# Optimization experiments

Hardware: AMD Instinct MI355X
Metric: run time of the kernel (lower is better)

The kernel has to match this reference:

```python
import jax, jax.numpy as jnp
from jax import lax
import numpy as np

K_LIST = [2, 4, 8]

def setup_inputs() -> dict:
    key = jax.random.key(0)
    k1, k2 = jax.random.split(key)
    B_, C, H, Wd = 8, 256, 128, 128
    x = jax.random.normal(k1, (B_, C, H, Wd), dtype=jnp.float32)
    # conv weights init ~ N(0, 1e-6) per the module's 'zero' init, bias zero
    W = jax.random.normal(k2, (len(K_LIST), 1, C, 3, 3), dtype=jnp.float32) * 1e-6
    Bb = jnp.zeros((len(K_LIST), 1), dtype=jnp.float32)
    return {"x": x, "W": W, "B": Bb}


def _band_grid(h, w):
    # signed max of (fftfreq_h, rfftfreq_w) coords, matching torch code
    fh = jnp.fft.fftfreq(h).astype(jnp.float32)          # [h]
    fw = jnp.fft.rfftfreq(w).astype(jnp.float32)         # [w//2+1]
    return jnp.maximum(fh[:, None], fw[None, :])         # [h, w//2+1]


def reference(x, W, B):
    b, c, h, w = x.shape
    x_dtype = x.dtype
    x32 = x.astype(jnp.float32)
    x_fft = jnp.fft.rfft2(x32, norm='ortho')             # [b,c,h,w//2+1] complex
    grid = _band_grid(h, w)
    pre_x = x32
    out = jnp.zeros_like(x32)
    for idx, freq in enumerate(K_LIST):
        mask = (grid < 0.5 / freq).astype(jnp.float32)   # [h, w//2+1]
        low = jnp.fft.irfft2(x_fft * mask, s=(h, w), norm='ortho')
        high = pre_x - low
        pre_x = low
        # Conv2d(in=256, out=1, k=3, pad=1) on att_feat=x
        fwgt = lax.conv_general_dilated(
            x32, W[idx], window_strides=(1, 1), padding='SAME',
            dimension_numbers=('NCHW', 'OIHW', 'NCHW'))
        fwgt = fwgt + B[idx][None, :, None, None]        # [b,1,h,w]
        gate = jax.nn.sigmoid(fwgt) * 2.0
        out = out + gate * high                          # broadcast over channels
    out = out + pre_x                                    # residual low-frequency part
    return out.astype(x_dtype)
```

## Files before the change

kernel.cpp:

```cpp
#include <hip/hip_runtime.h>


#define NPIX 16384
#define NCHN 256

typedef __attribute__((ext_vector_type(8))) short bf16x8;
typedef __attribute__((ext_vector_type(4))) float f32x4;

__device__ __align__(16) short g_f[64][128];
__device__ __align__(16) short g_h[192][256];
__device__ __align__(16) short g_e[3][256][192];
__device__ __align__(16) short g_p[3][128][64];

static __device__ __forceinline__ short f2bf(float f) {
  unsigned u = __float_as_uint(f);
  unsigned r = (u + 0x7fffu + ((u >> 16) & 1u)) >> 16;
  return (short)r;
}
static __device__ __forceinline__ float bf2f(short s) {
  return __uint_as_float(((unsigned)(unsigned short)s) << 16);
}
static __device__ __forceinline__ f32x4 mfma16(bf16x8 a, bf16x8 b, f32x4 c) {
  return __builtin_amdgcn_mfma_f32_16x16x32_bf16(a, b, c, 0, 0, 0);
}

static __device__ void const_fill(int idx) {
  const float C = 6.2831853071795864769f / 128.f;
  if (idx < 8192) {
    int n = idx >> 7, q = idx & 127;
    int j = n & 31;
    float ang = C * (float)((j * q) & 127);
    float v = (n < 32) ? cosf(ang) : -sinf(ang);
    reinterpret_cast<short*>(g_f)[idx] = f2bf(v);
  } else if (idx < 57344) {
    int e = idx - 8192;
    int d = e >> 8, kk = e & 255;
    int r = (d < 96) ? d : d - 96;
    int ifr = (r < 32) ? r : r + 32;
    float ang = C * (float)((ifr * (kk & 127)) & 127);
    float cv = cosf(ang) * (1.f / 128.f), sv = sinf(ang) * (1.f / 128.f);
    float v = (d < 96) ? ((kk < 128) ? cv : sv) : ((kk < 128) ? -sv : cv);
    reinterpret_cast<short*>(g_h)[e] = f2bf(v);
  } else if (idx < 204800) {
    int e = idx - 57344;
    int k = e / 49152; int e2 = e % 49152;
    int mm = e2 / 192, kk = e2 % 192;
    int nk = 32 >> k;
    int r = (kk < 96) ? kk : kk - 96;
    bool allow = (r < nk) || (r >= 32);
    int ifr = (r < 32) ? r : r + 32;
    float ang = C * (float)((ifr * (mm & 127)) & 127);
    float cv = cosf(ang), sv = sinf(ang);
    float v = (mm < 128) ? ((kk < 96) ? cv : -sv) : ((kk < 96) ? sv : cv);
    reinterpret_cast<short*>(g_e)[e] = f2bf(allow ? v : 0.f);
  } else if (idx < 229376) {
    int e = idx - 204800;
    int k = e / 8192; int e2 = e % 8192;
    int n = e2 >> 6, jj = e2 & 63;
    int nk = 32 >> k;
    int j = jj & 31;
    bool valid = (j < nk) && (jj < 32 || j > 0);
    float wj = (j == 0) ? (1.f / 128.f) : (2.f / 128.f);
    float ang = C * (float)((j * n) & 127);
    float v = (jj < 32) ? (wj * cosf(ang)) : (-wj * sinf(ang));
    reinterpret_cast<short*>(g_p)[e] = f2bf(valid ? v : 0.f);
  }
}

__global__ __launch_bounds__(256) void gates_partial_kernel(
    const float* __restrict__ x, const float* __restrict__ Wg,
    float* __restrict__ partial, int nsplit) {
  int bid = blockIdx.x;
  int ngates = 512 * nsplit;
  if (bid >= ngates) {
    const_fill((bid - ngates) * 256 + threadIdx.x);
    return;
  }
  int b = bid & 7;
  int tile = (bid >> 3) & 63;
  int cs = bid >> 9;
  int chans = NCHN / nsplit;
  int m = ((tile >> 3) << 4) + (threadIdx.x >> 4);
  int n = ((tile & 7) << 4) + (threadIdx.x & 15);
  float a0 = 0.f, a1 = 0.f, a2 = 0.f;
  const float* xb = x + (size_t)b * NCHN * NPIX;
  for (int c = cs * chans; c < cs * chans + chans; ++c) {
    const float* xc = xb + (size_t)c * NPIX;
    const float* wc = Wg + c * 9;
    #pragma unroll
    for (int dh = -1; dh <= 1; ++dh) {
      int gm = m + dh;
      bool vm = (unsigned)gm < 128u;
      #pragma unroll
      for (int dw = -1; dw <= 1; ++dw) {
        int gn = n + dw;
        float xv = (vm && (unsigned)gn < 128u) ? xc[gm * 128 + gn] : 0.f;
        int tap = (dh + 1) * 3 + (dw + 1);
        a0 = fmaf(xv, wc[tap], a0);
        a1 = fmaf(xv, wc[2304 + tap], a1);
        a2 = fmaf(xv, wc[4608 + tap], a2);
      }
    }
  }
  int pix = m * 128 + n;
  float* pp = partial + (size_t)(cs * 8 + b) * 3 * NPIX;
  pp[pix]            = a0;
  pp[NPIX + pix]     = a1;
  pp[2 * NPIX + pix] = a2;
}

__global__ __launch_bounds__(256) void gates_combine_kernel(
    const float* __restrict__ partial, const float* __restrict__ Bg,
    short* __restrict__ dcoef, int nsplit) {
  int bid = blockIdx.x;
  int b = bid & 7;
  int px = (bid >> 3) * 256 + threadIdx.x;
  float a0 = Bg[0], a1 = Bg[1], a2 = Bg[2];
  for (int cs = 0; cs < nsplit; ++cs) {
    const float* pp = partial + (size_t)(cs * 8 + b) * 3 * NPIX;
    a0 += pp[px];
    a1 += pp[NPIX + px];
    a2 += pp[2 * NPIX + px];
  }
  float g1 = 2.f / (1.f + expf(-a0));
  float g2 = 2.f / (1.f + expf(-a1));
  float g3 = 2.f / (1.f + expf(-a2));
  int pix = b * NPIX + px;
  dcoef[pix]          = f2bf(g1 - 1.f);
  dcoef[131072 + pix] = f2bf(g2 - g1);
  dcoef[262144 + pix] = f2bf(g3 - g2);
  dcoef[393216 + pix] = f2bf(1.f - g3);
}

__global__ __launch_bounds__(256) void gates_kernel(
    const float* __restrict__ x, const float* __restrict__ Wg,
    const float* __restrict__ Bg, short* __restrict__ dcoef) {
  int blk = blockIdx.x;
  if (blk >= 512) {
    const_fill((blk - 512) * 256 + threadIdx.x);
    return;
  }
  int b = blk >> 6;
  int tile = blk & 63;
  int m = ((tile >> 3) << 4) + (threadIdx.x >> 4);
  int n = ((tile & 7) << 4) + (threadIdx.x & 15);
  float a0 = 0.f, a1 = 0.f, a2 = 0.f;
  const float* xb = x + (size_t)b * NCHN * NPIX;
  for (int c = 0; c < NCHN; ++c) {
    const float* xc = xb + (size_t)c * NPIX;
    const float* wc = Wg + c * 9;
    #pragma unroll
    for (int dh = -1; dh <= 1; ++dh) {
      int gm = m + dh;
      bool vm = (unsigned)gm < 128u;
      #pragma unroll
      for (int dw = -1; dw <= 1; ++dw) {
        int gn = n + dw;
        float xv = (vm && (unsigned)gn < 128u) ? xc[gm * 128 + gn] : 0.f;
        int tap = (dh + 1) * 3 + (dw + 1);
        a0 = fmaf(xv, wc[tap], a0);
        a1 = fmaf(xv, wc[2304 + tap], a1);
        a2 = fmaf(xv, wc[4608 + tap], a2);
      }
    }
  }
  a0 += Bg[0]; a1 += Bg[1]; a2 += Bg[2];
  float g1 = 2.f / (1.f + expf(-a0));
  float g2 = 2.f / (1.f + expf(-a1));
  float g3 = 2.f / (1.f + expf(-a2));
  int pix = b * NPIX + m * 128 + n;
  dcoef[pix]          = f2bf(g1 - 1.f);
  dcoef[131072 + pix] = f2bf(g2 - g1);
  dcoef[262144 + pix] = f2bf(g3 - g2);
  dcoef[393216 + pix] = f2bf(1.f - g3);
}

__global__ __launch_bounds__(512, 2) void fbm_kernel(
    const float* __restrict__ x, const short* __restrict__ dcoef,
    float* __restrict__ out) {
  __shared__ __align__(16) short Xs[16384];
  __shared__ __align__(16) short WVs[8192];
  __shared__ __align__(16) short Ds2[6144];
  char* XsB = reinterpret_cast<char*>(Xs);
  char* PlaneB = XsB;
  char* WsB = reinterpret_cast<char*>(WVs);
  char* DsB = reinterpret_cast<char*>(Ds2);

  int t = threadIdx.x;
  int bid = blockIdx.x;
  int b = bid >> 5;
  int cg = bid & 31;
  size_t img0 = ((size_t)b << 8) + ((size_t)cg << 3);
  int lane = t & 63, w = t >> 6;
  int l15 = lane & 15, l4 = lane >> 4;
  const f32x4 zero = {0.f, 0.f, 0.f, 0.f};

  const short4* d0p = reinterpret_cast<const short4*>(dcoef + ((size_t)b << 14));

  for (int c = 0; c < 8; ++c) {
    f32x4 oaccC[8];
    {
      const f32x4* xv4 = reinterpret_cast<const f32x4*>(x + (img0 + c) * NPIX);
      #pragma unroll
      for (int i = 0; i < 8; ++i) {
        int f = t + i * 512;
        f32x4 xv = __builtin_nontemporal_load(&xv4[f]);
        short4 dv = d0p[f];
        f32x4 dvf = {bf2f(dv.x), bf2f(dv.y), bf2f(dv.z), bf2f(dv.w)};
        oaccC[i] = xv + dvf * xv;
        int row = f >> 5;
        int byte = row * 256 + (((f & 31) * 8) ^ ((row & 7) << 4));
        short4 s;
        s.x = f2bf(xv[0]); s.y = f2bf(xv[1]); s.z = f2bf(xv[2]); s.w = f2bf(xv[3]);
        *reinterpret_cast<short4*>(XsB + byte) = s;
      }
    }
    __syncthreads();

    {
      int Ntile = w & 3, Mq = w >> 2;
      int n = Ntile * 16 + l15;
      f32x4 acc[4] = {zero, zero, zero, zero};
      #pragma unroll
      for (int ks = 0; ks < 4; ++ks) {
        int koff = ks * 32 + l4 * 8;
        bf16x8 bf = *reinterpret_cast<const bf16x8*>(&g_f[n][koff]);
        #pragma unroll
        for (int mt = 0; mt < 4; ++mt) {
          int p = (Mq * 4 + mt) * 16 + l15;
          bf16x8 a = *reinterpret_cast<const bf16x8*>(
              XsB + p * 256 + ((koff * 2) ^ ((p & 7) << 4)));
          acc[mt] = mfma16(a, bf, acc[mt]);
        }
      }
      #pragma unroll
      for (int mt = 0; mt < 4; ++mt) {
        int p0 = (Mq * 4 + mt) * 16 + l4 * 4;
        short4 s;
        s.x = f2bf(acc[mt][0]); s.y = f2bf(acc[mt][1]);
        s.z = f2bf(acc[mt][2]); s.w = f2bf(acc[mt][3]);
        *reinterpret_cast<short4*>(WsB + n * 256 + ((p0 * 2) ^ ((n & 7) << 4))) = s;
      }
    }
    __syncthreads();

    {
      int Ntile = w & 1, Mt3 = w >> 1;
      int n = Ntile * 16 + l15;
      f32x4 acc[3] = {zero, zero, zero};
      #pragma unroll
      for (int ks = 0; ks < 8; ++ks) {
        int koff = ks * 32 + l4 * 8;
        int wrow = n + ((ks >= 4) ? 32 : 0);
        bf16x8 bb = *reinterpret_cast<const bf16x8*>(
            WsB + wrow * 256 + (((koff & 127) * 2) ^ ((wrow & 7) << 4)));
        #pragma unroll
        for (int mt = 0; mt < 3; ++mt) {
          int d = (Mt3 * 3 + mt) * 16 + l15;
          bf16x8 aa = *reinterpret_cast<const bf16x8*>(&g_h[d][koff]);
          acc[mt] = mfma16(aa, bb, acc[mt]);
        }
      }
      #pragma unroll
      for (int mt = 0; mt < 3; ++mt) {
        int d0 = (Mt3 * 3 + mt) * 16 + l4 * 4;
        short4 s;
        s.x = f2bf(acc[mt][0]); s.y = f2bf(acc[mt][1]);
        s.z = f2bf(acc[mt][2]); s.w = f2bf(acc[mt][3]);
        *reinterpret_cast<short4*>(DsB + n * 384 + ((d0 * 2) ^ ((n & 7) << 4))) = s;
      }
    }
    __syncthreads();

    int Mg3 = w >> 2, Ng3 = w & 3;
    for (int k = 0; k < 3; ++k) {
      {
        f32x4 acc[2][2] = {{zero, zero}, {zero, zero}};
        #pragma unroll
        for (int ks = 0; ks < 6; ++ks) {
          int koff = ks * 32 + l4 * 8;
          bf16x8 b0 = *reinterpret_cast<const bf16x8*>(
              DsB + l15 * 384 + ((koff * 2) ^ ((l15 & 7) << 4)));
          int j1 = 16 + l15;
          bf16x8 b1 = *reinterpret_cast<const bf16x8*>(
              DsB + j1 * 384 + ((koff * 2) ^ ((j1 & 7) << 4)));
          #pragma unroll
          for (int mi = 0; mi < 2; ++mi) {
            int mstk = (2 * w + mi) * 16 + l15;
            bf16x8 aa = *reinterpret_cast<const bf16x8*>(&g_e[k][mstk][koff]);
            acc[mi][0] = mfma16(aa, b0, acc[mi][0]);
            acc[mi][1] = mfma16(aa, b1, acc[mi][1]);
          }
        }
        #pragma unroll
        for (int mi = 0; mi < 2; ++mi) {
          #pragma unroll
          for (int ni = 0; ni < 2; ++ni) {
            int j = ni * 16 + l15;
            #pragma unroll
            for (int r = 0; r < 4; ++r) {
              int mstk = (2 * w + mi) * 16 + l4 * 4 + r;
              int m = mstk & 127;
              int jst = ((mstk >> 7) << 5) + j;
              *reinterpret_cast<short*>(WsB + m * 128 + ((jst * 2) ^ ((m & 7) << 4))) =
                  f2bf(acc[mi][ni][r]);
            }
          }
        }
      }
      __syncthreads();
      {
        f32x4 acc[4][2] = {{zero, zero}, {zero, zero}, {zero, zero}, {zero, zero}};
        #pragma unroll
        for (int ks = 0; ks < 2; ++ks) {
          int koff = ks * 32 + l4 * 8;
          bf16x8 bfr[2];
          #pragma unroll
          for (int nt = 0; nt < 2; ++nt) {
            int nout = (Ng3 * 2 + nt) * 16 + l15;
            bfr[nt] = *reinterpret_cast<const bf16x8*>(&g_p[k][nout][koff]);
          }
          #pragma unroll
          for (int mt = 0; mt < 4; ++mt) {
            int m = (Mg3 * 4 + mt) * 16 + l15;
            bf16x8 aa = *reinterpret_cast<const bf16x8*>(
                WsB + m * 128 + ((koff * 2) ^ ((m & 7) << 4)));
            acc[mt][0] = mfma16(aa, bfr[0], acc[mt][0]);
            acc[mt][1] = mfma16(aa, bfr[1], acc[mt][1]);
          }
        }
        #pragma unroll
        for (int mt = 0; mt < 4; ++mt) {
          #pragma unroll
          for (int nt = 0; nt < 2; ++nt) {
            int col = (Ng3 * 2 + nt) * 16 + l15;
            #pragma unroll
            for (int r = 0; r < 4; ++r) {
              int row = (Mg3 * 4 + mt) * 16 + l4 * 4 + r;
              int byte = row * 256 + ((col ^ ((row & 7) << 2)) << 1);
              *reinterpret_cast<short*>(PlaneB + byte) = f2bf(acc[mt][nt][r]);
            }
          }
        }
      }
      __syncthreads();
      {
        const short4* dk = reinterpret_cast<const short4*>(
            dcoef + (size_t)(k + 1) * 131072 + ((size_t)b << 14));
        #pragma unroll
        for (int i = 0; i < 8; ++i) {
          int f = t + i * 512;
          int row = f >> 5;
          int col = (f & 31) * 4;
          int byte = row * 256 + ((col ^ ((row & 7) << 2)) << 1);
          short4 s = *reinterpret_cast<const short4*>(PlaneB + byte);
          short4 dv = dk[f];
          oaccC[i][0] = fmaf(bf2f(dv.x), bf2f(s.x), oaccC[i][0]);
          oaccC[i][1] = fmaf(bf2f(dv.y), bf2f(s.y), oaccC[i][1]);
          oaccC[i][2] = fmaf(bf2f(dv.z), bf2f(s.z), oaccC[i][2]);
          oaccC[i][3] = fmaf(bf2f(dv.w), bf2f(s.w), oaccC[i][3]);
        }
      }
    }
    __syncthreads();

    f32x4* og4 = reinterpret_cast<f32x4*>(out + (img0 + c) * NPIX);
    #pragma unroll
    for (int i = 0; i < 8; ++i) og4[t + i * 512] = oaccC[i];
  }
}

extern "C" void kernel_launch(void* const* d_in, const int* in_sizes, int n_in,
                              void* d_out, int out_size, void* d_ws, size_t ws_size,
                              hipStream_t stream) {
  const float* x  = (const float*)d_in[0];
  const float* Wg = (const float*)d_in[1];
  const float* Bg = (const float*)d_in[2];
  float* out  = (float*)d_out;
  short* dcoef = (short*)d_ws;
  float* partial = (float*)((char*)d_ws + (1u << 20));
  size_t need8 = (1u << 20) + (size_t)8 * 8 * 3 * NPIX * 4;
  if (ws_size >= need8) {
    gates_partial_kernel<<<4096 + 896, 256, 0, stream>>>(x, Wg, partial, 8);
    gates_combine_kernel<<<512, 256, 0, stream>>>(partial, Bg, dcoef, 8);
  } else if (ws_size >= (size_t)(8u << 20)) {
    gates_partial_kernel<<<2048 + 896, 256, 0, stream>>>(x, Wg, partial, 4);
    gates_combine_kernel<<<512, 256, 0, stream>>>(partial, Bg, dcoef, 4);
  } else {
    gates_kernel<<<1408, 256, 0, stream>>>(x, Wg, Bg, dcoef);
  }
  fbm_kernel<<<256, 512, 0, stream>>>(x, dcoef, out);
}
```

Baseline: 305.3 us.

## Process two channel images concurrently per block with split LDS buffers

The block is split into two 4-wave groups, each with its own set of shared-memory buffers, so two channel images are handled per iteration instead of one. This halves the number of outer iterations and their barriers. Each wave now covers twice the tile work. Per-pixel gate coefficients are folded into the last GEMM epilogue, which accumulates a bf16 band sum in the X plane instead of keeping fp32 accumulators in registers. The input is re-read at the end to form the output, and that output is written with nontemporal stores. In exchange, LDS use doubles, which may limit the two-blocks-per-CU occupancy. The global input is read twice, and accumulating in bf16 adds rounding error.

```diff
diff --git a/kernel.cpp b/kernel.cpp
--- a/kernel.cpp
+++ b/kernel.cpp
@@ -178,13 +178,9 @@
 __global__ __launch_bounds__(512, 2) void fbm_kernel(
     const float* __restrict__ x, const short* __restrict__ dcoef,
     float* __restrict__ out) {
-  __shared__ __align__(16) short Xs[16384];
-  __shared__ __align__(16) short WVs[8192];
-  __shared__ __align__(16) short Ds2[6144];
-  char* XsB = reinterpret_cast<char*>(Xs);
-  char* PlaneB = XsB;
-  char* WsB = reinterpret_cast<char*>(WVs);
-  char* DsB = reinterpret_cast<char*>(Ds2);
+  __shared__ __align__(16) short Xs0[16384], Xs1[16384];
+  __shared__ __align__(16) short WV0[8192], WV1[8192];
+  __shared__ __align__(16) short Ds0[6144], Ds1[6144];
 
   int t = threadIdx.x;
   int bid = blockIdx.x;
@@ -192,60 +188,69 @@
   int cg = bid & 31;
   size_t img0 = ((size_t)b << 8) + ((size_t)cg << 3);
   int lane = t & 63, w = t >> 6;
+  int g = w >> 2, wg = w & 3;
+  int tg = t & 255;
   int l15 = lane & 15, l4 = lane >> 4;
   const f32x4 zero = {0.f, 0.f, 0.f, 0.f};
 
-  const short4* d0p = reinterpret_cast<const short4*>(dcoef + ((size_t)b << 14));
-
-  for (int c = 0; c < 8; ++c) {
-    f32x4 oaccC[8];
+  char* XP = reinterpret_cast<char*>(g ? Xs1 : Xs0);
+  char* WP = reinterpret_cast<char*>(g ? WV1 : WV0);
+  char* DP = reinterpret_cast<char*>(g ? Ds1 : Ds0);
+
+  const short* dbase = dcoef + ((size_t)b << 14);
+  const short4* d0p = reinterpret_cast<const short4*>(dbase);
+
+  for (int pair = 0; pair < 4; ++pair) {
+    size_t img = img0 + pair * 2 + g;
+
     {
-      const f32x4* xv4 = reinterpret_cast<const f32x4*>(x + (img0 + c) * NPIX);
-      #pragma unroll
-      for (int i = 0; i < 8; ++i) {
-        int f = t + i * 512;
+      const f32x4* xv4 = reinterpret_cast<const f32x4*>(x + img * NPIX);
+      #pragma unroll
+      for (int i = 0; i < 16; ++i) {
+        int f = tg + i * 256;
         f32x4 xv = __builtin_nontemporal_load(&xv4[f]);
-        short4 dv = d0p[f];
-        f32x4 dvf = {bf2f(dv.x), bf2f(dv.y), bf2f(dv.z), bf2f(dv.w)};
-        oaccC[i] = xv + dvf * xv;
         int row = f >> 5;
         int byte = row * 256 + (((f & 31) * 8) ^ ((row & 7) << 4));
         short4 s;
         s.x = f2bf(xv[0]); s.y = f2bf(xv[1]); s.z = f2bf(xv[2]); s.w = f2bf(xv[3]);
-        *reinterpret_cast<short4*>(XsB + byte) = s;
+        *reinterpret_cast<short4*>(XP + byte) = s;
       }
     }
     __syncthreads();
 
     {
-      int Ntile = w & 3, Mq = w >> 2;
-      int n = Ntile * 16 + l15;
-      f32x4 acc[4] = {zero, zero, zero, zero};
-      #pragma unroll
-      for (int ks = 0; ks < 4; ++ks) {
-        int koff = ks * 32 + l4 * 8;
-        bf16x8 bf = *reinterpret_cast<const bf16x8*>(&g_f[n][koff]);
+      int n = wg * 16 + l15;
+      #pragma unroll
+      for (int h = 0; h < 2; ++h) {
+        f32x4 acc[4] = {zero, zero, zero, zero};
+        #pragma unroll
+        for (int ks = 0; ks < 4; ++ks) {
+          int koff = ks * 32 + l4 * 8;
+          bf16x8 bf = *reinterpret_cast<const bf16x8*>(&g_f[n][koff]);
+          #pragma unroll
+          for (int mt = 0; mt < 4; ++mt) {
+            int p = (h * 4 + mt) * 16 + l15;
+            bf16x8 a = *reinterpret_cast<const bf16x8*>(
+                XP + p * 256 + ((koff * 2) ^ ((p & 7) << 4)));
+            acc[mt] = mfma16(a, bf, acc[mt]);
+          }
+        }
         #pragma unroll
         for (int mt = 0; mt < 4; ++mt) {
-          int p = (Mq * 4 + mt) * 16 + l15;
-          bf16x8 a = *reinterpret_cast<const bf16x8*>(
-              XsB + p * 256 + ((koff * 2) ^ ((p & 7) << 4)));
-          acc[mt] = mfma16(a, bf, acc[mt]);
-        }
-      }
-      #pragma unroll
-      for (int mt = 0; mt < 4; ++mt) {
-        int p0 = (Mq * 4 + mt) * 16 + l4 * 4;
-        short4 s;
-        s.x = f2bf(acc[mt][0]); s.y = f2bf(acc[mt][1]);
-        s.z = f2bf(acc[mt][2]); s.w = f2bf(acc[mt][3]);
-        *reinterpret_cast<short4*>(WsB + n * 256 + ((p0 * 2) ^ ((n & 7) << 4))) = s;
+          int p0 = (h * 4 + mt) * 16 + l4 * 4;
+          short4 s;
+          s.x = f2bf(acc[mt][0]); s.y = f2bf(acc[mt][1]);
+          s.z = f2bf(acc[mt][2]); s.w = f2bf(acc[mt][3]);
+          *reinterpret_cast<short4*>(WP + n * 256 + ((p0 * 2) ^ ((n & 7) << 4))) = s;
+        }
       }
     }
     __syncthreads();
 
-    {
-      int Ntile = w & 1, Mt3 = w >> 1;
+    #pragma unroll
+    for (int h = 0; h < 2; ++h) {
+      int wv = wg + 4 * h;
+      int Ntile = wv & 1, Mt3 = wv >> 1;
       int n = Ntile * 16 + l15;
       f32x4 acc[3] = {zero, zero, zero};
       #pragma unroll
@@ -253,7 +258,7 @@
         int koff = ks * 32 + l4 * 8;
         int wrow = n + ((ks >= 4) ? 32 : 0);
         bf16x8 bb = *reinterpret_cast<const bf16x8*>(
-            WsB + wrow * 256 + (((koff & 127) * 2) ^ ((wrow & 7) << 4)));
+            WP + wrow * 256 + (((koff & 127) * 2) ^ ((wrow & 7) << 4)));
         #pragma unroll
         for (int mt = 0; mt < 3; ++mt) {
           int d = (Mt3 * 3 + mt) * 16 + l15;
@@ -267,26 +272,27 @@
         short4 s;
         s.x = f2bf(acc[mt][0]); s.y = f2bf(acc[mt][1]);
         s.z = f2bf(acc[mt][2]); s.w = f2bf(acc[mt][3]);
-        *reinterpret_cast<short4*>(DsB + n * 384 + ((d0 * 2) ^ ((n & 7) << 4))) = s;
+        *reinterpret_cast<short4*>(DP + n * 384 + ((d0 * 2) ^ ((n & 7) << 4))) = s;
       }
     }
     __syncthreads();
 
-    int Mg3 = w >> 2, Ng3 = w & 3;
     for (int k = 0; k < 3; ++k) {
-      {
+      #pragma unroll
+      for (int h = 0; h < 2; ++h) {
+        int wv = wg + 4 * h;
         f32x4 acc[2][2] = {{zero, zero}, {zero, zero}};
         #pragma unroll
         for (int ks = 0; ks < 6; ++ks) {
           int koff = ks * 32 + l4 * 8;
           bf16x8 b0 = *reinterpret_cast<const bf16x8*>(
-              DsB + l15 * 384 + ((koff * 2) ^ ((l15 & 7) << 4)));
+              DP + l15 * 384 + ((koff * 2) ^ ((l15 & 7) << 4)));
           int j1 = 16 + l15;
           bf16x8 b1 = *reinterpret_cast<const bf16x8*>(
-              DsB + j1 * 384 + ((koff * 2) ^ ((j1 & 7) << 4)));
+              DP + j1 * 384 + ((koff * 2) ^ ((j1 & 7) << 4)));
           #pragma unroll
           for (int mi = 0; mi < 2; ++mi) {
-            int mstk = (2 * w + mi) * 16 + l15;
+            int mstk = (2 * wv + mi) * 16 + l15;
             bf16x8 aa = *reinterpret_cast<const bf16x8*>(&g_e[k][mstk][koff]);
             acc[mi][0] = mfma16(aa, b0, acc[mi][0]);
             acc[mi][1] = mfma16(aa, b1, acc[mi][1]);
@@ -299,10 +305,10 @@
             int j = ni * 16 + l15;
             #pragma unroll
             for (int r = 0; r < 4; ++r) {
-              int mstk = (2 * w + mi) * 16 + l4 * 4 + r;
+              int mstk = (2 * wv + mi) * 16 + l4 * 4 + r;
               int m = mstk & 127;
               int jst = ((mstk >> 7) << 5) + j;
-              *reinterpret_cast<short*>(WsB + m * 128 + ((jst * 2) ^ ((m & 7) << 4))) =
+              *reinterpret_cast<short*>(WP + m * 128 + ((jst * 2) ^ ((m & 7) << 4))) =
                   f2bf(acc[mi][ni][r]);
             }
           }
@@ -310,63 +316,71 @@
       }
       __syncthreads();
       {
-        f32x4 acc[4][2] = {{zero, zero}, {zero, zero}, {zero, zero}, {zero, zero}};
-        #pragma unroll
-        for (int ks = 0; ks < 2; ++ks) {
-          int koff = ks * 32 + l4 * 8;
-          bf16x8 bfr[2];
+        const short* dkp = dbase + (size_t)(k + 1) * 131072;
+        #pragma unroll
+        for (int h = 0; h < 2; ++h) {
+          int Mg3 = h, Ng3 = wg;
+          f32x4 acc[4][2] = {{zero, zero}, {zero, zero}, {zero, zero}, {zero, zero}};
           #pragma unroll
-          for (int nt = 0; nt < 2; ++nt) {
-            int nout = (Ng3 * 2 + nt) * 16 + l15;
-            bfr[nt] = *reinterpret_cast<const bf16x8*>(&g_p[k][nout][koff]);
+          for (int ks = 0; ks < 2; ++ks) {
+            int koff = ks * 32 + l4 * 8;
+            bf16x8 bfr[2];
+            #pragma unroll
+            for (int nt = 0; nt < 2; ++nt) {
+              int nout = (Ng3 * 2 + nt) * 16 + l15;
+              bfr[nt] = *reinterpret_cast<const bf16x8*>(&g_p[k][nout][koff]);
+            }
+            #pragma unroll
+            for (int mt = 0; mt < 4; ++mt) {
+              int m = (Mg3 * 4 + mt) * 16 + l15;
+              bf16x8 aa = *reinterpret_cast<const bf16x8*>(
+                  WP + m * 128 + ((koff * 2) ^ ((m & 7) << 4)));
+              acc[mt][0] = mfma16(aa, bfr[0], acc[mt][0]);
+              acc[mt][1] = mfma16(aa, bfr[1], acc[mt][1]);
+            }
           }
           #pragma unroll
           for (int mt = 0; mt < 4; ++mt) {
-            int m = (Mg3 * 4 + mt) * 16 + l15;
-            bf16x8 aa = *reinterpret_cast<const bf16x8*>(
-                WsB + m * 128 + ((koff * 2) ^ ((m & 7) << 4)));
-            acc[mt][0] = mfma16(aa, bfr[0], acc[mt][0]);
-            acc[mt][1] = mfma16(aa, bfr[1], acc[mt][1]);
-          }
-        }
-        #pragma unroll
-        for (int mt = 0; mt < 4; ++mt) {
-          #pragma unroll
-          for (int nt = 0; nt < 2; ++nt) {
-            int col = (Ng3 * 2 + nt) * 16 + l15;
             #pragma unroll
-            for (int r = 0; r < 4; ++r) {
-              int row = (Mg3 * 4 + mt) * 16 + l4 * 4 + r;
-              int byte = row * 256 + ((col ^ ((row & 7) << 2)) << 1);
-              *reinterpret_cast<short*>(PlaneB + byte) = f2bf(acc[mt][nt][r]);
+            for (int nt = 0; nt < 2; ++nt) {
+              int col = (Ng3 * 2 + nt) * 16 + l15;
+              #pragma unroll
+              for (int r = 0; r < 4; ++r) {
+                int row = (Mg3 * 4 + mt) * 16 + l4 * 4 + r;
+                float dv = bf2f(dkp[row * 128 + col]);
+                int byte = row * 256 + ((col ^ ((row & 7) << 2)) << 1);
+                short* ap = reinterpret_cast<short*>(XP + byte);
+                float prev = (k == 0) ? 0.f : bf2f(*ap);
+                *ap = f2bf(fmaf(dv, acc[mt][nt][r], prev));
+              }
             }
           }
         }
       }
       __syncthreads();
-      {
-        const short4* dk = reinterpret_cast<const short4*>(
-            dcoef + (size_t)(k + 1) * 131072 + ((size_t)b << 14));
-        #pragma unroll
-        for (int i = 0; i < 8; ++i) {
-          int f = t + i * 512;
-          int row = f >> 5;
-          int col = (f & 31) * 4;
-          int byte = row * 256 + ((col ^ ((row & 7) << 2)) << 1);
-          short4 s = *reinterpret_cast<const short4*>(PlaneB + byte);
-          short4 dv = dk[f];
-          oaccC[i][0] = fmaf(bf2f(dv.x), bf2f(s.x), oaccC[i][0]);
-          oaccC[i][1] = fmaf(bf2f(dv.y), bf2f(s.y), oaccC[i][1]);
-          oaccC[i][2] = fmaf(bf2f(dv.z), bf2f(s.z), oaccC[i][2]);
-          oaccC[i][3] = fmaf(bf2f(dv.w), bf2f(s.w), oaccC[i][3]);
-        }
+    }
+
+    {
+      const f32x4* xv4 = reinterpret_cast<const f32x4*>(x + img * NPIX);
+      f32x4* og4 = reinterpret_cast<f32x4*>(out + img * NPIX);
+      #pragma unroll
+      for (int i = 0; i < 16; ++i) {
+        int f = tg + i * 256;
+        f32x4 xv = xv4[f];
+        short4 dv = d0p[f];
+        int row = f >> 5;
+        int col = (f & 31) * 4;
+        int byte = row * 256 + ((col ^ ((row & 7) << 2)) << 1);
+        short4 s = *reinterpret_cast<const short4*>(XP + byte);
+        f32x4 o;
+        o[0] = fmaf(bf2f(dv.x), xv[0], xv[0]) + bf2f(s.x);
+        o[1] = fmaf(bf2f(dv.y), xv[1], xv[1]) + bf2f(s.y);
+        o[2] = fmaf(bf2f(dv.z), xv[2], xv[2]) + bf2f(s.z);
+        o[3] = fmaf(bf2f(dv.w), xv[3], xv[3]) + bf2f(s.w);
+        __builtin_nontemporal_store(o, &og4[f]);
       }
     }
     __syncthreads();
-
-    f32x4* og4 = reinterpret_cast<f32x4*>(out + (img0 + c) * NPIX);
-    #pragma unroll
-    for (int i = 0; i < 8; ++i) og4[t + i * 512] = oaccC[i];
   }
 }
 
```

Result: slower. 514.1 us (+68.4%).
